# Performance work log

Measured on AMD Instinct MI355X. Metric: run time of the kernel, lower is better.

The kernel has to match this reference:

```python
import jax, jax.numpy as jnp
import numpy as np

D_MODEL = 512; D_STATE = 64; D_CONV = 4; EXPAND = 1; HEADDIM = 128; NGROUPS = 2; CHUNK = 256
D_INNER = EXPAND * (D_MODEL // 2)          # 256
NHEADS = D_INNER // HEADDIM                 # 2
CONV_DIM = D_INNER + 2 * NGROUPS * D_STATE  # 512
D_IN_PROJ = CONV_DIM + NHEADS               # 514

def silu(x):
    return x * jax.nn.sigmoid(x)

def conv1x1(x, w, b):
    # x: (b,c,h,w), w: (o,c)
    return jnp.einsum('bchw,oc->bohw', x, w) + b[None, :, None, None]

def dwconv3x3(x, w, b):
    # depthwise 3x3, SAME padding; w: (c,1,3,3)
    c = x.shape[1]
    y = jax.lax.conv_general_dilated(x, w, (1, 1), 'SAME', feature_group_count=c,
                                     dimension_numbers=('NCHW', 'OIHW', 'NCHW'))
    return y + b[None, :, None, None]

def causal_dwconv1d(x, w, b):
    # x: (b,L,c); w: (c,k). Torch pads k-1 both sides then slices [:L] -> causal left pad.
    k = w.shape[1]
    xp = jnp.pad(x, ((0, 0), (k - 1, 0), (0, 0))).transpose(0, 2, 1)  # (b,c,L+k-1)
    y = jax.lax.conv_general_dilated(xp, w[:, None, :], (1,), 'VALID',
                                     feature_group_count=w.shape[0],
                                     dimension_numbers=('NCH', 'OIH', 'NCH'))
    return y.transpose(0, 2, 1) + b

def axis_attn(x, qw, qb, fw, fb, axis):
    # DualAxisAggAttn single-axis step
    qkv = conv1x1(x, qw, qb)
    c = x.shape[1]
    q, k, v = qkv[:, :1], qkv[:, 1:1 + c], qkv[:, 1 + c:]
    dim = -1 if axis == 'W' else -2
    scores = jax.nn.softmax(q, axis=dim)
    ctx = jnp.sum(k * scores, axis=dim, keepdims=True)
    out = x + jax.nn.sigmoid(v) * ctx
    return conv1x1(out, fw, fb)

def segsum(x):
    # x: (...,T) -> (...,T,T) lower-triangular segment sums, -inf above diagonal
    T = x.shape[-1]
    cs = jnp.cumsum(x, -1)
    d = cs[..., :, None] - cs[..., None, :]
    mask = jnp.tril(jnp.ones((T, T), bool))
    return jnp.where(mask, d, -jnp.inf)

def ssd(X, A, B, C, chunk):
    # Mamba2 SSD chunked scan. X: (b,l,h,p) = x*dt; A: (b,l,h) = dt*A_head; B,C: (b,l,h,n)
    b, l, h, p = X.shape; n = B.shape[-1]; c = l // chunk
    X = X.reshape(b, c, chunk, h, p)
    B = B.reshape(b, c, chunk, h, n)
    C = C.reshape(b, c, chunk, h, n)
    A = A.reshape(b, c, chunk, h).transpose(0, 3, 1, 2)  # (b,h,c,L)
    Acs = jnp.cumsum(A, -1)
    L = jnp.exp(segsum(A))  # (b,h,c,L,L) intra-chunk decay
    Yd = jnp.einsum('bclhn,bcshn,bhcls,bcshp->bclhp', C, B, L, X)
    dec = jnp.exp(Acs[..., -1:] - Acs)
    st = jnp.einsum('bclhn,bhcl,bclhp->bchpn', B, dec, X)  # chunk end-states
    st = jnp.concatenate([jnp.zeros_like(st[:, :1]), st], 1)
    dchunk = jnp.exp(segsum(jnp.pad(Acs[..., -1], ((0, 0), (0, 0), (1, 0)))))
    st = jnp.einsum('bhzc,bchpn->bzhpn', dchunk, st)[:, :-1]  # states entering each chunk
    Yo = jnp.einsum('bclhn,bchpn,bhcl->bclhp', C, st, jnp.exp(Acs))
    return (Yd + Yo).reshape(b, l, h, p)

def setup_inputs() -> dict:
    key = jax.random.key(0)
    ks = jax.random.split(key, 12)
    s = 0.02
    p = {}
    p['u'] = jax.random.normal(ks[0], (8, D_MODEL, 64, 64), jnp.float32)
    p['sc_w1'] = jax.random.normal(ks[1], (D_MODEL, D_MODEL)) * s
    p['sc_b1'] = jnp.zeros((D_MODEL,))
    p['sc_wdw'] = jax.random.normal(ks[2], (D_MODEL, 1, 3, 3)) * s
    p['sc_bdw'] = jnp.zeros((D_MODEL,))
    p['sc_w2'] = jax.random.normal(ks[3], (D_INNER, D_MODEL)) * s
    p['sc_b2'] = jnp.zeros((D_INNER,))
    p['mc_w'] = jax.random.normal(ks[4], (D_INNER, D_MODEL)) * s
    p['mc_b'] = jnp.zeros((D_INNER,))
    p['qkvW_w'] = jax.random.normal(ks[5], (1 + 2 * D_INNER, D_INNER)) * s
    p['qkvW_b'] = jnp.zeros((1 + 2 * D_INNER,))
    p['qkvH_w'] = jax.random.normal(ks[6], (1 + 2 * D_INNER, D_INNER)) * s
    p['qkvH_b'] = jnp.zeros((1 + 2 * D_INNER,))
    p['fuseW_w'] = jax.random.normal(ks[7], (D_INNER, D_INNER)) * s
    p['fuseW_b'] = jnp.zeros((D_INNER,))
    p['fuseH_w'] = jax.random.normal(ks[8], (D_INNER, D_INNER)) * s
    p['fuseH_b'] = jnp.zeros((D_INNER,))
    p['in_proj_w'] = jax.random.normal(ks[9], (D_IN_PROJ, D_INNER)) * s
    p['conv1d_w'] = jax.random.normal(ks[10], (CONV_DIM, D_CONV)) * s
    p['conv1d_b'] = jnp.zeros((CONV_DIM,))
    dt = np.exp(np.linspace(np.log(1e-3), np.log(0.1), NHEADS))
    p['dt_bias'] = jnp.asarray(dt + np.log(-np.expm1(-dt)), jnp.float32)
    p['A_log'] = jnp.asarray(np.log(np.linspace(1.0, 16.0, NHEADS)), jnp.float32)
    p['D'] = jnp.ones((NHEADS,))
    p['norm_w'] = jnp.ones((D_INNER,))
    p['outp_w'] = jax.random.normal(ks[11], (D_MODEL, 2 * D_INNER)) * s
    p['outp_b'] = jnp.zeros((D_MODEL,))
    return p

def reference(u, sc_w1, sc_b1, sc_wdw, sc_bdw, sc_w2, sc_b2, mc_w, mc_b,
              qkvW_w, qkvW_b, qkvH_w, qkvH_b, fuseW_w, fuseW_b, fuseH_w, fuseH_b,
              in_proj_w, conv1d_w, conv1d_b, dt_bias, A_log, D, norm_w, outp_w, outp_b):
    b, _, H, W = u.shape
    # short_conv branch (light_ConvBlock: 1x1 -> dw3x3 -> 1x1, all SiLU; BN folded into bias)
    z = silu(conv1x1(u, sc_w1, sc_b1))
    z = silu(dwconv3x3(z, sc_wdw, sc_bdw))
    z = silu(conv1x1(z, sc_w2, sc_b2))
    # main branch
    x = silu(conv1x1(u, mc_w, mc_b))
    x = axis_attn(x, qkvW_w, qkvW_b, fuseW_w, fuseW_b, 'W')
    x = axis_attn(x, qkvH_w, qkvH_b, fuseH_w, fuseH_b, 'H')
    seqlen = H * W
    u2 = x.transpose(0, 2, 3, 1).reshape(b, seqlen, D_INNER)  # b (h w) c
    xbcdt = u2 @ in_proj_w.T  # (b,l,d_in_proj)
    xBC = xbcdt[..., :CONV_DIM]
    dt = jax.nn.softplus(xbcdt[..., CONV_DIM:] + dt_bias)  # (b,l,h)
    A = -jnp.exp(A_log)  # (h,)
    xBC = silu(causal_dwconv1d(xBC, conv1d_w, conv1d_b))
    xs = xBC[..., :D_INNER]
    Bs = xBC[..., D_INNER:D_INNER + NGROUPS * D_STATE].reshape(b, seqlen, NGROUPS, D_STATE)
    Cs = xBC[..., D_INNER + NGROUPS * D_STATE:].reshape(b, seqlen, NGROUPS, D_STATE)
    Xh = xs.reshape(b, seqlen, NHEADS, HEADDIM)
    rep = NHEADS // NGROUPS
    Bh = jnp.repeat(Bs, rep, axis=2)
    Ch = jnp.repeat(Cs, rep, axis=2)
    y = ssd(Xh * dt[..., None], dt * A[None, None, :], Bh, Ch, CHUNK)
    y = y + Xh * D[None, None, :, None]  # D skip connection
    y = y.reshape(b, seqlen, D_INNER)
    # RMSNormGated with z=None -> plain RMSNorm
    y = y * jax.lax.rsqrt(jnp.mean(y * y, -1, keepdims=True) + 1e-5) * norm_w
    y = y.reshape(b, H, W, D_INNER).transpose(0, 3, 1, 2)
    y = jnp.concatenate([z, y], axis=1)
    return conv1x1(y, outp_w, outp_b)
```

## Files before the change

kernel.cpp:

```cpp
#include <hip/hip_runtime.h>
#include <hip/hip_bf16.h>
#include <cstddef>
#include <cstdint>

#define PTOT 32768
#define HWSZ 4096

typedef __attribute__((ext_vector_type(8))) short bf16x8;
typedef __attribute__((ext_vector_type(4))) short s16x4;
typedef __attribute__((ext_vector_type(4))) float f32x4;

__device__ __forceinline__ float sigf(float x){ return 1.f/(1.f+__expf(-x)); }
__device__ __forceinline__ float siluf(float x){ return x*sigf(x); }
__device__ __forceinline__ short f2b(float x){
  __hip_bfloat16 h = __float2bfloat16(x);
  return *reinterpret_cast<short*>(&h);
}
__device__ __forceinline__ float b2f(short s){
  unsigned u = ((unsigned)(unsigned short)s) << 16;
  return __uint_as_float(u);
}

__device__ __forceinline__ void gload16(const void* g, void* l){
  __builtin_amdgcn_global_load_lds(
      (const __attribute__((address_space(1))) unsigned int*)g,
      (__attribute__((address_space(3))) unsigned int*)l, 16, 0, 0);
}

__global__ __launch_bounds__(256) void k_cvtw(
    const float* __restrict__ s0, const float* __restrict__ s1, const float* __restrict__ s2,
    const float* __restrict__ s3, const float* __restrict__ s4,
    short* __restrict__ dst){
  int idx = blockIdx.x*256 + threadIdx.x;
  const float* s; int off;
  if      (idx <  262144){ s=s0; off=idx; }
  else if (idx <  393216){ s=s1; off=idx- 262144; }
  else if (idx <  524288){ s=s2; off=idx- 393216; }
  else if (idx <  655616){ s=s3; off=idx- 524288; }
  else if (idx <  917760){ s=s4; off=idx- 655616; }
  else return;
  dst[idx] = f2b(s[off]);
}

__global__ __launch_bounds__(256) void k_wcomp(
    const float* __restrict__ qkvHw, const float* __restrict__ fuWw,
    const float* __restrict__ fuWb,  const float* __restrict__ qkvHb,
    const float* __restrict__ inpw,  const float* __restrict__ fuHw,
    const float* __restrict__ fuHb,
    const float* __restrict__ scb1,  const float* __restrict__ mcb,
    short* __restrict__ wcomb, float* __restrict__ bcomb,
    short* __restrict__ wi2,   float* __restrict__ bi2,
    short* __restrict__ wqH,   short* __restrict__ wdt,
    float* __restrict__ bzx)
{
  int blk = blockIdx.x;
  int tid = threadIdx.x;
  __shared__ float as[256];
  __shared__ float red[256];
  if (blk < 513){
    int i = blk;
    int r = (i==512) ? 0 : (i+1);
    as[tid]  = qkvHw[(size_t)r*256 + tid];
    red[tid] = as[tid] * fuWb[tid];
    __syncthreads();
    for (int off=128; off; off>>=1){ if (tid<off) red[tid]+=red[tid+off]; __syncthreads(); }
    float acc = 0.f;
    #pragma unroll 8
    for (int k=0;k<256;k++) acc += as[k]*fuWw[(size_t)k*256 + tid];
    if (i < 512){
      wcomb[(size_t)(256+i)*256 + tid] = f2b(acc);
      if (tid==0) bcomb[256+i] = red[0] + qkvHb[r];
    } else {
      wqH[tid] = f2b(acc);
      if (tid==0) bcomb[768] = red[0] + qkvHb[0];
    }
  } else if (blk < 769){
    int j = blk - 513;
    wcomb[(size_t)j*256 + tid] = f2b(fuWw[(size_t)j*256 + tid]);
    if (tid==0) bcomb[j] = fuWb[j];
  } else if (blk < 1283){
    int j = blk - 769;
    as[tid]  = inpw[(size_t)j*256 + tid];
    red[tid] = as[tid] * fuHb[tid];
    __syncthreads();
    for (int off=128; off; off>>=1){ if (tid<off) red[tid]+=red[tid+off]; __syncthreads(); }
    float acc = 0.f;
    #pragma unroll 8
    for (int k=0;k<256;k++) acc += as[k]*fuHw[(size_t)k*256 + tid];
    if (j < 512){
      wi2[(size_t)j*256 + tid] = f2b(acc);
      if (tid==0) bi2[j] = red[0];
    } else {
      wdt[(size_t)(j-512)*256 + tid] = f2b(acc);
      if (tid==0) bi2[j] = red[0];
    }
  } else {
    int j = (blk - 1283)*256 + tid;
    bzx[j] = (j < 512) ? scb1[j] : mcb[j-512];
  }
}

__global__ __launch_bounds__(256) void k_transpose(const float* __restrict__ in, short* __restrict__ out){
  __shared__ float tile[64][33];
  int b = blockIdx.z;
  int c0 = blockIdx.y * 64;
  int s0 = blockIdx.x * 32;
  int tx = threadIdx.x, ty = threadIdx.y;
  const float* ip = in + ((size_t)b*512 + c0)*HWSZ + s0;
  for (int i = ty; i < 64; i += 8) tile[i][tx] = ip[(size_t)i*HWSZ + tx];
  __syncthreads();
  for (int i = ty; i < 32; i += 8){
    unsigned lo = (unsigned)(unsigned short)f2b(tile[2*tx][i]);
    unsigned hi = (unsigned)(unsigned short)f2b(tile[2*tx+1][i]);
    unsigned pk = lo | (hi<<16);
    *reinterpret_cast<unsigned*>(&out[((size_t)((b<<12) + s0 + i))*512 + c0 + 2*tx]) = pk;
  }
}

template<int ACT, int OUT_NCHW>
__global__ __launch_bounds__(256) void k_gemm(
    const short* __restrict__ A0, const short* __restrict__ A1,
    int kSplit, int lda0, int lda1,
    const short* __restrict__ Wt, const float* __restrict__ bias,
    void* __restrict__ Cpv, int N, int K, int ldc, int qkvPerm,
    short* __restrict__ Cp2, int nSplit2, int ldc2)
{
  __shared__ char arena[17408];
  short* Alds = (short*)arena;
  short* Wlds = (short*)(arena + 8192);

  int tid = threadIdx.x;
  int lane = tid & 63;
  int wv = tid >> 6;
  int wr = wv >> 1, wc = wv & 1;
  int lr = lane & 15, lh = lane >> 4;
  int bm = blockIdx.x * 128;
  int bn = blockIdx.y * 128;

  int rl = lane >> 2;
  int kg = (lane & 3) << 3;

  const short* aB0[2];
  const short* aB1[2];
  const short* wB[2];
  #pragma unroll
  for (int j=0;j<2;j++){
    int r = wv*32 + j*16 + rl;
    int m = bm + r;
    aB0[j] = A0 + (size_t)m*lda0 + kg;
    aB1[j] = A1 + (size_t)m*lda1 + kg;
    int n = bn + r; if (n > N-1) n = N-1;
    int wn = qkvPerm ? (n+1) : n;
    wB[j] = Wt + (size_t)wn*K + kg;
  }

  f32x4 acc[4][4];
  #pragma unroll
  for (int i=0;i<4;i++)
    #pragma unroll
    for (int j=0;j<4;j++) acc[i][j] = (f32x4){0.f,0.f,0.f,0.f};

  for (int k0 = 0; k0 < K; k0 += 32){
    {
      const short* s0;
      const short* s1;
      if (k0 < kSplit){ s0 = aB0[0] + k0; s1 = aB0[1] + k0; }
      else            { s0 = aB1[0] + (k0 - kSplit); s1 = aB1[1] + (k0 - kSplit); }
      gload16(s0, &Alds[(wv*32)*32]);
      gload16(s1, &Alds[(wv*32 + 16)*32]);
      gload16(wB[0] + k0, &Wlds[(wv*32)*32]);
      gload16(wB[1] + k0, &Wlds[(wv*32 + 16)*32]);
    }
    __syncthreads();
    bf16x8 af[4], bfr[4];
    #pragma unroll
    for (int mi=0;mi<4;mi++)
      af[mi] = *reinterpret_cast<const bf16x8*>(&Alds[(wr*64 + mi*16 + lr)*32 + lh*8]);
    #pragma unroll
    for (int ni=0;ni<4;ni++)
      bfr[ni] = *reinterpret_cast<const bf16x8*>(&Wlds[(wc*64 + ni*16 + lr)*32 + lh*8]);
    #pragma unroll
    for (int mi=0;mi<4;mi++)
      #pragma unroll
      for (int ni=0;ni<4;ni++)
        acc[mi][ni] = __builtin_amdgcn_mfma_f32_16x16x32_bf16(af[mi], bfr[ni], acc[mi][ni], 0, 0, 0);
    __syncthreads();
  }

  if (!OUT_NCHW){
    short* Cp = (short*)Cpv;
    #pragma unroll
    for (int mi=0;mi<4;mi++){
      int m = bm + wr*64 + mi*16 + lh*4;
      #pragma unroll
      for (int ni=0;ni<4;ni++){
        int n = bn + wc*64 + ni*16 + lr;
        if (n < N){
          int wn = qkvPerm ? (n+1) : n;
          float bb = bias ? bias[wn] : 0.f;
          #pragma unroll
          for (int r=0;r<4;r++){
            float v = acc[mi][ni][r] + bb;
            if (ACT==1) v = siluf(v);
            short sv = f2b(v);
            if (n < nSplit2) Cp[(size_t)(m+r)*ldc + n] = sv;
            else             Cp2[(size_t)(m+r)*ldc2 + (n - nSplit2)] = sv;
          }
        }
      }
    }
  } else {
    float* Cp = (float*)Cpv;
    float* Sep = ((float*)arena) + wv*16*68;
    #pragma unroll
    for (int mi=0;mi<4;mi++){
      __syncthreads();
      #pragma unroll
      for (int ni=0;ni<4;ni++){
        int n = bn + wc*64 + ni*16 + lr;
        float bb = (bias && n < N) ? bias[n] : 0.f;
        #pragma unroll
        for (int r=0;r<4;r++){
          float v = acc[mi][ni][r] + bb;
          if (ACT==1) v = siluf(v);
          Sep[(lh*4+r)*68 + ni*16 + lr] = v;
        }
      }
      __syncthreads();
      int m = bm + wr*64 + mi*16 + lr;
      size_t mb = ((size_t)(m>>12)*ldc)*HWSZ + (m & 4095);
      #pragma unroll
      for (int g=0; g<16; g++){
        int nl = g*4 + lh;
        float v = Sep[lr*68 + nl];
        int nn = bn + wc*64 + nl;
        if (nn < N) Cp[mb + (size_t)nn*HWSZ] = v;
      }
    }
  }
}

__global__ __launch_bounds__(256) void k_dwconv3x3(const short* __restrict__ in,
    const float* __restrict__ w, const float* __restrict__ bias, short* __restrict__ out){
  int tid = threadIdx.x;
  int cq = tid & 127;
  int wi = tid >> 7;
  int bw = blockIdx.x;
  int b  = bw >> 5;
  int wc = ((bw & 31) << 1) | wi;
  int h0 = blockIdx.y << 4;
  int c  = cq << 2;

  float arr[36];
  {
    const float* wp = &w[c*9];
    #pragma unroll
    for (int t=0;t<9;t++){
      f32x4 v = *reinterpret_cast<const f32x4*>(wp + t*4);
      arr[t*4+0]=v[0]; arr[t*4+1]=v[1]; arr[t*4+2]=v[2]; arr[t*4+3]=v[3];
    }
  }
  f32x4 bias4 = *reinterpret_cast<const f32x4*>(&bias[c]);

  int pb = b << 12;
  auto ldrow = [&](int r, int dw)->f32x4 {
    int ww = wc + dw;
    if ((unsigned)r >= 64u || (unsigned)ww >= 64u) return (f32x4){0.f,0.f,0.f,0.f};
    s16x4 v = *reinterpret_cast<const s16x4*>(&in[((size_t)(pb + (r<<6) + ww) << 9) + c]);
    return (f32x4){b2f(v[0]), b2f(v[1]), b2f(v[2]), b2f(v[3])};
  };

  f32x4 a00,a01,a02,a10,a11,a12,a20,a21,a22;
  a00=ldrow(h0-1,-1); a01=ldrow(h0-1,0); a02=ldrow(h0-1,1);
  a10=ldrow(h0  ,-1); a11=ldrow(h0  ,0); a12=ldrow(h0  ,1);
  #pragma unroll
  for (int hh=0; hh<16; hh++){
    int h = h0 + hh;
    a20=ldrow(h+1,-1); a21=ldrow(h+1,0); a22=ldrow(h+1,1);
    s16x4 o;
    #pragma unroll
    for (int j=0;j<4;j++){
      float v = bias4[j];
      v = fmaf(a00[j], arr[j*9+0], v);
      v = fmaf(a01[j], arr[j*9+1], v);
      v = fmaf(a02[j], arr[j*9+2], v);
      v = fmaf(a10[j], arr[j*9+3], v);
      v = fmaf(a11[j], arr[j*9+4], v);
      v = fmaf(a12[j], arr[j*9+5], v);
      v = fmaf(a20[j], arr[j*9+6], v);
      v = fmaf(a21[j], arr[j*9+7], v);
      v = fmaf(a22[j], arr[j*9+8], v);
      o[j] = f2b(siluf(v));
    }
    *reinterpret_cast<s16x4*>(&out[((size_t)(pb + (h<<6) + wc) << 9) + c]) = o;
    a00=a10; a01=a11; a02=a12;
    a10=a20; a11=a21; a12=a22;
  }
}

__global__ __launch_bounds__(256) void k_attn_ctx(
    const short* __restrict__ xq, int xqld, const short* __restrict__ wq, const float* __restrict__ bq,
    const short* __restrict__ qkv, int qld, int kOff,
    float* __restrict__ ctx, int axisH){
  int bl = blockIdx.x;
  int b = bl >> 6, line = bl & 63;
  int tid = threadIdx.x;
  int pbase = b << 12;
  __shared__ float qs[64], es[64];
  __shared__ float qpart[4][64];
  __shared__ float part[8][260];
  auto pos = [&](int t)->int { return axisH ? (pbase | (t<<6) | line) : (pbase | (line<<6) | t); };
  {
    int t = tid & 63, qr = tid >> 6;
    const short* xp = &xq[(size_t)pos(t)*xqld + qr*64];
    const short* wp = &wq[qr*64];
    float pq = 0.f;
    #pragma unroll
    for (int j=0;j<8;j++){
      bf16x8 xv = *reinterpret_cast<const bf16x8*>(xp + j*8);
      bf16x8 wv = *reinterpret_cast<const bf16x8*>(wp + j*8);
      #pragma unroll
      for (int e=0;e<8;e++) pq = fmaf(b2f(xv[e]), b2f(wv[e]), pq);
    }
    qpart[qr][t] = pq;
  }
  __syncthreads();
  if (tid < 64) qs[tid] = bq[0] + qpart[0][tid] + qpart[1][tid] + qpart[2][tid] + qpart[3][tid];
  __syncthreads();
  float mx = -1e30f;
  for (int t=0;t<64;t++) mx = fmaxf(mx, qs[t]);
  if (tid < 64) es[tid] = __expf(qs[tid]-mx);
  __syncthreads();
  int tg = tid >> 5;
  int cg = tid & 31;
  float pacc[8];
  #pragma unroll
  for (int j=0;j<8;j++) pacc[j]=0.f;
  #pragma unroll
  for (int tt=0; tt<8; tt++){
    int t = tg*8 + tt;
    bf16x8 kv = *reinterpret_cast<const bf16x8*>(&qkv[(size_t)pos(t)*qld + kOff + cg*8]);
    float e = es[t];
    #pragma unroll
    for (int j=0;j<8;j++) pacc[j] = fmaf(e, b2f(kv[j]), pacc[j]);
  }
  #pragma unroll
  for (int j=0;j<8;j++) part[tg][cg*8+j] = pacc[j];
  __syncthreads();
  float s = 0.f;
  for (int t=0;t<64;t++) s += es[t];
  float inv = 1.f/s;
  int c = tid;
  float v = 0.f;
  #pragma unroll
  for (int g=0; g<8; g++) v += part[g][c];
  ctx[(size_t)bl*256 + c] = v*inv;
}

__global__ __launch_bounds__(256) void k_attn_apply(const short* __restrict__ x, int xld,
    const short* __restrict__ qkv, int qld, int vOff, const float* __restrict__ ctx,
    short* __restrict__ out, int axisH){
  int idx = blockIdx.x*256 + threadIdx.x;
  int p = idx >> 5;
  int c0 = (idx & 31) << 3;
  int line = axisH ? (p & 63) : ((p >> 6) & 63);
  int bl = (p >> 12)*64 + line;
  bf16x8 vv = *reinterpret_cast<const bf16x8*>(&qkv[(size_t)p*qld + vOff + c0]);
  bf16x8 xv = *reinterpret_cast<const bf16x8*>(&x[(size_t)p*xld + c0]);
  const float* cp = &ctx[(size_t)bl*256 + c0];
  bf16x8 o;
  #pragma unroll
  for (int j=0;j<8;j++)
    o[j] = f2b(b2f(xv[j]) + sigf(b2f(vv[j]))*cp[j]);
  *reinterpret_cast<bf16x8*>(&out[(size_t)p*256 + c0]) = o;
}

__global__ __launch_bounds__(256) void k_dt(const short* __restrict__ xwh,
    const short* __restrict__ wdt, const float* __restrict__ bdt,
    const float* __restrict__ dt_bias, float* __restrict__ dtb){
  int tid = threadIdx.x, lane = tid & 63, wv = tid >> 6;
  int p = blockIdx.x*4 + wv;
  s16x4 xv = *reinterpret_cast<const s16x4*>(&xwh[(size_t)p*256 + lane*4]);
  s16x4 w0 = *reinterpret_cast<const s16x4*>(&wdt[lane*4]);
  s16x4 w1 = *reinterpret_cast<const s16x4*>(&wdt[256 + lane*4]);
  float d0 = 0.f, d1 = 0.f;
  #pragma unroll
  for (int j=0;j<4;j++){
    float xf = b2f(xv[j]);
    d0 = fmaf(xf, b2f(w0[j]), d0);
    d1 = fmaf(xf, b2f(w1[j]), d1);
  }
  #pragma unroll
  for (int off=32; off; off>>=1){ d0 += __shfl_down(d0, off); d1 += __shfl_down(d1, off); }
  if (lane == 0){
    float x0 = d0 + bdt[0] + dt_bias[0];
    float x1 = d1 + bdt[1] + dt_bias[1];
    dtb[(size_t)p*2 + 0] = (x0 > 20.f) ? x0 : log1pf(__expf(x0));
    dtb[(size_t)p*2 + 1] = (x1 > 20.f) ? x1 : log1pf(__expf(x1));
  }
}

__global__ __launch_bounds__(256) void k_conv1d(const short* __restrict__ xbc_in,
    const float* __restrict__ w, const float* __restrict__ bias, short* __restrict__ xBC){
  int tid = threadIdx.x;
  int cq = tid & 127;
  int c  = cq << 2;
  int half = tid >> 7;
  int bs = blockIdx.x;
  int b  = bs >> 7;
  int t0 = ((((bs & 127) << 1) | half) << 4);

  float wk[16];
  {
    const float* wp = &w[c*4];
    #pragma unroll
    for (int t=0;t<4;t++){
      f32x4 v = *reinterpret_cast<const f32x4*>(wp + t*4);
      wk[t*4+0]=v[0]; wk[t*4+1]=v[1]; wk[t*4+2]=v[2]; wk[t*4+3]=v[3];
    }
  }
  f32x4 bias4 = *reinterpret_cast<const f32x4*>(&bias[c]);

  int pb = b << 12;
  auto ld = [&](int t)->f32x4 {
    if (t < 0) return (f32x4){0.f,0.f,0.f,0.f};
    s16x4 v = *reinterpret_cast<const s16x4*>(&xbc_in[((size_t)(pb + t) << 9) + c]);
    return (f32x4){b2f(v[0]), b2f(v[1]), b2f(v[2]), b2f(v[3])};
  };

  f32x4 x0,x1,x2,x3;
  x0 = ld(t0-3); x1 = ld(t0-2); x2 = ld(t0-1);
  #pragma unroll
  for (int tt=0; tt<16; tt++){
    int t = t0 + tt;
    x3 = ld(t);
    s16x4 o;
    #pragma unroll
    for (int j=0;j<4;j++){
      float v = bias4[j];
      v = fmaf(x0[j], wk[j*4+0], v);
      v = fmaf(x1[j], wk[j*4+1], v);
      v = fmaf(x2[j], wk[j*4+2], v);
      v = fmaf(x3[j], wk[j*4+3], v);
      o[j] = f2b(siluf(v));
    }
    *reinterpret_cast<s16x4*>(&xBC[((size_t)(pb + t) << 9) + c]) = o;
    x0=x1; x1=x2; x2=x3;
  }
}

__global__ __launch_bounds__(256) void k_ssd_states(
  const short* __restrict__ xBC, const float* __restrict__ dtb, const float* __restrict__ A_log,
  float* __restrict__ states, float* __restrict__ AcsG, float* __restrict__ AtotG)
{
  int ci = blockIdx.x, h = blockIdx.y, b = blockIdx.z;
  int tid = threadIdx.x, lane = tid & 63, wv = tid >> 6;
  int lg = lane >> 4, lr = lane & 15;
  __shared__ float sa[256], sb[256];
  __shared__ short Bt[64*72];
  __shared__ short Xt[128*72];
  int base = (b<<12) | (ci<<8);
  float Ah = -__expf(A_log[h]);
  sa[tid] = dtb[(size_t)(base + tid)*2 + h] * Ah;
  __syncthreads();
  float* src = sa; float* dst = sb;
  for (int off=1; off<256; off<<=1){
    float v = src[tid];
    if (tid >= off) v += src[tid - off];
    dst[tid] = v;
    __syncthreads();
    float* tswap = src; src = dst; dst = tswap;
  }
  float acs = src[tid];
  float atot = src[255];
  AcsG[((size_t)((b*2+h)*16 + ci))*256 + tid] = acs;
  if (tid == 0) AtotG[(b*2+h)*16 + ci] = atot;

  f32x4 acc[8];
  #pragma unroll
  for (int pf=0;pf<8;pf++) acc[pf] = (f32x4){0.f,0.f,0.f,0.f};

  for (int t0=0; t0<256; t0+=64){
    __syncthreads();
    {
      int t = tid >> 2;
      int n0 = (tid & 3) << 4;
      float d = __expf(atot - src[t0 + t]);
      const short* sp = &xBC[(size_t)(base + t0 + t)*512 + 256 + (h<<6) + n0];
      bf16x8 v0 = *reinterpret_cast<const bf16x8*>(sp);
      bf16x8 v1 = *reinterpret_cast<const bf16x8*>(sp+8);
      #pragma unroll
      for (int e=0;e<8;e++) Bt[(n0+e)*72 + t]   = f2b(b2f(v0[e])*d);
      #pragma unroll
      for (int e=0;e<8;e++) Bt[(n0+8+e)*72 + t] = f2b(b2f(v1[e])*d);
    }
    {
      int t = tid >> 2;
      int p0 = (tid & 3) << 5;
      float dtv = dtb[(size_t)(base + t0 + t)*2 + h];
      const short* sp = &xBC[(size_t)(base + t0 + t)*512 + (h<<7) + p0];
      #pragma unroll
      for (int q=0;q<4;q++){
        bf16x8 v = *reinterpret_cast<const bf16x8*>(sp + q*8);
        #pragma unroll
        for (int e=0;e<8;e++) Xt[(p0 + q*8 + e)*72 + t] = f2b(b2f(v[e])*dtv);
      }
    }
    __syncthreads();
    #pragma unroll
    for (int kk=0; kk<2; kk++){
      bf16x8 af = *reinterpret_cast<const bf16x8*>(&Bt[(wv*16 + lr)*72 + kk*32 + lg*8]);
      #pragma unroll
      for (int pf=0;pf<8;pf++){
        bf16x8 xf = *reinterpret_cast<const bf16x8*>(&Xt[(pf*16 + lr)*72 + kk*32 + lg*8]);
        acc[pf] = __builtin_amdgcn_mfma_f32_16x16x32_bf16(af, xf, acc[pf], 0, 0, 0);
      }
    }
  }
  float* stp = states + (((size_t)(b*16+ci)*2 + h) << 13);
  #pragma unroll
  for (int pf=0;pf<8;pf++){
    #pragma unroll
    for (int r=0;r<4;r++)
      stp[(wv*16 + lg*4 + r)*128 + pf*16 + lr] = acc[pf][r];
  }
}

__global__ __launch_bounds__(256) void k_ssd_scan(const float* __restrict__ states,
    const float* __restrict__ AtotG, float* __restrict__ R){
  int bh = blockIdx.x;
  int b = bh >> 1, h = bh & 1;
  int tid = threadIdx.x;
  float r[32];
  #pragma unroll
  for (int j=0;j<32;j++) r[j]=0.f;
  for (int ci=0; ci<16; ci++){
    size_t off = (((size_t)(b*16+ci)*2) + h) << 13;
    #pragma unroll
    for (int j=0;j<32;j++) R[off + tid + (j<<8)] = r[j];
    if (ci < 15){
      float sc = __expf(AtotG[bh*16 + ci]);
      #pragma unroll
      for (int j=0;j<32;j++) r[j] = fmaf(sc, r[j], states[off + tid + (j<<8)]);
    }
  }
}

__global__ __launch_bounds__(256) void k_ssd_y_norm(
  const short* __restrict__ xBC, const float* __restrict__ dtb,
  const float* __restrict__ AcsG, const float* __restrict__ R,
  const float* __restrict__ Dp, const float* __restrict__ nw, short* __restrict__ ynorm)
{
// ... 61 lines not shown
        bf16x8 bb0 = *reinterpret_cast<const bf16x8*>(&Bbf[(f*16+lr)*72 + lg*8]);
        bf16x8 bb1 = *reinterpret_cast<const bf16x8*>(&Bbf[(f*16+lr)*72 + 32 + lg*8]);
        sacc[f] = __builtin_amdgcn_mfma_f32_16x16x32_bf16(ca0, bb0, sacc[f], 0, 0, 0);
        sacc[f] = __builtin_amdgcn_mfma_f32_16x16x32_bf16(ca1, bb1, sacc[f], 0, 0, 0);
      }
      #pragma unroll
      for (int f=0;f<4;f++){
        #pragma unroll
        for (int r=0;r<4;r++){
          int ll = w*16 + lg*4 + r;
          int ss = f*16 + lr;
          float v = 0.f;
          if (s0 + ss <= l0 + ll)
            v = sacc[f][r] * __expf(acs_l[ll] - acs_s[ss]) * dt_s[ss];
          Sbf[ll*72 + ss] = f2b(v);
        }
      }
      __syncthreads();

      bf16x8 sa0 = *reinterpret_cast<const bf16x8*>(&Sbf[(w*16+lr)*72 + lg*8]);
      bf16x8 sa1 = *reinterpret_cast<const bf16x8*>(&Sbf[(w*16+lr)*72 + 32 + lg*8]);
      #pragma unroll
      for (int pf=0;pf<8;pf++){
        bf16x8 x0 = *reinterpret_cast<const bf16x8*>(&Xt[(pf*16+lr)*76 + lg*8]);
        bf16x8 x1 = *reinterpret_cast<const bf16x8*>(&Xt[(pf*16+lr)*76 + 32 + lg*8]);
        yacc[pf] = __builtin_amdgcn_mfma_f32_16x16x32_bf16(sa0, x0, yacc[pf], 0, 0, 0);
        yacc[pf] = __builtin_amdgcn_mfma_f32_16x16x32_bf16(sa1, x1, yacc[pf], 0, 0, 0);
      }
    }

    __syncthreads();
    {
      size_t roff = (((size_t)(b*16+ci)*2) + h) << 13;
      int n = tid >> 2;
      const float* src = R + roff + (size_t)n*128;
      #pragma unroll
      for (int j=0;j<8;j++){
        int p = ((tid & 3) << 2) + (j << 4);
        float4 f = *reinterpret_cast<const float4*>(&src[p]);
        Xt[(p+0)*76 + n] = f2b(f.x);
        Xt[(p+1)*76 + n] = f2b(f.y);
        Xt[(p+2)*76 + n] = f2b(f.z);
        Xt[(p+3)*76 + n] = f2b(f.w);
      }
    }
    __syncthreads();
    f32x4 racc[8];
    #pragma unroll
    for (int pf=0;pf<8;pf++) racc[pf] = (f32x4){0.f,0.f,0.f,0.f};
    {
      bf16x8 ca0 = *reinterpret_cast<const bf16x8*>(&Cbf[(w*16+lr)*72 + lg*8]);
      bf16x8 ca1 = *reinterpret_cast<const bf16x8*>(&Cbf[(w*16+lr)*72 + 32 + lg*8]);
      #pragma unroll
      for (int pf=0;pf<8;pf++){
        bf16x8 x0 = *reinterpret_cast<const bf16x8*>(&Xt[(pf*16+lr)*76 + lg*8]);
        bf16x8 x1 = *reinterpret_cast<const bf16x8*>(&Xt[(pf*16+lr)*76 + 32 + lg*8]);
        racc[pf] = __builtin_amdgcn_mfma_f32_16x16x32_bf16(ca0, x0, racc[pf], 0, 0, 0);
        racc[pf] = __builtin_amdgcn_mfma_f32_16x16x32_bf16(ca1, x1, racc[pf], 0, 0, 0);
      }
    }
    float Dh = Dp[h];
    float el[4];
    #pragma unroll
    for (int r=0;r<4;r++) el[r] = __expf(acs_l[w*16 + lg*4 + r]);
    #pragma unroll
    for (int pf=0;pf<8;pf++){
      f32x4 o;
      #pragma unroll
      for (int r=0;r<4;r++){
        int ll = w*16 + lg*4 + r;
        int p = pf*16 + lr;
        size_t pix = (size_t)(base + l0 + ll);
        float xraw = b2f(xBC[pix*512 + (h<<7) + p]);
        o[r] = yacc[pf][r] + el[r]*racc[pf][r] + Dh*xraw;
      }
      yv[pf] = o;
    }
  };

  f32x4 y0[8], y1[8];
  body(0, y0);
  body(1, y1);

  f32x4 ss = (f32x4){0.f,0.f,0.f,0.f};
  #pragma unroll
  for (int pf=0;pf<8;pf++){
    #pragma unroll
    for (int r=0;r<4;r++)
      ss[r] += y0[pf][r]*y0[pf][r] + y1[pf][r]*y1[pf][r];
  }
  #pragma unroll
  for (int m=1; m<16; m<<=1){
    #pragma unroll
    for (int r=0;r<4;r++) ss[r] += __shfl_xor(ss[r], m);
  }
  f32x4 scale;
  #pragma unroll
  for (int r=0;r<4;r++) scale[r] = rsqrtf(ss[r]*(1.f/256.f) + 1e-5f);

  #pragma unroll
  for (int pf=0;pf<8;pf++){
    float nw0 = nw[pf*16 + lr];
    float nw1 = nw[128 + pf*16 + lr];
    #pragma unroll
    for (int r=0;r<4;r++){
      size_t pix = (size_t)(base + l0 + w*16 + lg*4 + r);
      ynorm[pix*256 + pf*16 + lr]        = f2b(y0[pf][r]*scale[r]*nw0);
      ynorm[pix*256 + 128 + pf*16 + lr]  = f2b(y1[pf][r]*scale[r]*nw1);
    }
  }
}

extern "C" void kernel_launch(void* const* d_in, const int* in_sizes, int n_in,
                              void* d_out, int out_size, void* d_ws, size_t ws_size,
                              hipStream_t stream)
{
  (void)in_sizes; (void)n_in; (void)out_size; (void)ws_size;
  const float* u        = (const float*)d_in[0];
  const float* sc_w1    = (const float*)d_in[1];
  const float* sc_b1    = (const float*)d_in[2];
  const float* sc_wdw   = (const float*)d_in[3];
  const float* sc_bdw   = (const float*)d_in[4];
  const float* sc_w2    = (const float*)d_in[5];
  const float* sc_b2    = (const float*)d_in[6];
  const float* mc_w     = (const float*)d_in[7];
  const float* mc_b     = (const float*)d_in[8];
  const float* qkvW_w   = (const float*)d_in[9];
  const float* qkvW_b   = (const float*)d_in[10];
  const float* qkvH_w   = (const float*)d_in[11];
  const float* qkvH_b   = (const float*)d_in[12];
  const float* fuseW_w  = (const float*)d_in[13];
  const float* fuseW_b  = (const float*)d_in[14];
  const float* fuseH_w  = (const float*)d_in[15];
  const float* fuseH_b  = (const float*)d_in[16];
  const float* in_proj_w= (const float*)d_in[17];
  const float* conv1d_w = (const float*)d_in[18];
  const float* conv1d_b = (const float*)d_in[19];
  const float* dt_bias  = (const float*)d_in[20];
  const float* A_log    = (const float*)d_in[21];
  const float* Dp       = (const float*)d_in[22];
  const float* norm_w   = (const float*)d_in[23];
  const float* outp_w   = (const float*)d_in[24];
  const float* outp_b   = (const float*)d_in[25];

  char* wsb = (char*)d_ws;
  size_t off = 0;
  auto alloc = [&](size_t bytes){ void* p = wsb + off; off = (off + bytes + 255) & ~(size_t)255; return p; };
  short* wbf   = (short*)alloc((size_t)1247000*2);
  float* bcomb = (float*)alloc(769*4);
  float* bi2   = (float*)alloc(514*4);
  float* bzx   = (float*)alloc(768*4);
  short* slotB = (short*)alloc((size_t)PTOT*768*2);
  short* slotC = (short*)alloc((size_t)PTOT*512*2);
  short* slotZ = (short*)alloc((size_t)PTOT*256*2);
  short* slotE = (short*)alloc((size_t)PTOT*256*2);
  short* slotF = (short*)alloc((size_t)PTOT*256*2);
  float* slotS = (float*)alloc((size_t)4460000*4);

  float* dtb     = slotS;
  float* AcsG    = slotS + 65536;
  float* AtotG   = slotS + 131072;
  float* statesB = slotS + 131328;
  float* Rb      = slotS + 131328 + 2097152;
  float* ctxb    = slotS;
  short* ynorm   = slotE;
  short* xwh     = slotF;

  short* w_zx   = wbf + 0;
  short* w_sc2  = wbf + 393216;
  short* w_qkvW = wbf + 524288;
  short* w_outp = wbf + 655616;
  short* wcomb  = wbf + 917760;
  short* wi2    = wbf + 1114368;
  short* wqH    = wbf + 1245440;
  short* wdt    = wbf + 1245696;

  short* u_pm = (short*)d_out;
  float* out  = (float*)d_out;

  const int BIG = 1<<30;

  k_cvtw<<<3585, 256, 0, stream>>>(sc_w1, mc_w, sc_w2, qkvW_w, outp_w, wbf);
  k_wcomp<<<1286, 256, 0, stream>>>(qkvH_w, fuseW_w, fuseW_b, qkvH_b, in_proj_w, fuseH_w, fuseH_b,
                                    sc_b1, mc_b, wcomb, bcomb, wi2, bi2, wqH, wdt, bzx);
  k_transpose<<<dim3(128,8,8), dim3(32,8), 0, stream>>>(u, u_pm);

  k_gemm<1,0><<<dim3(256,6), 256, 0, stream>>>(u_pm, u_pm, BIG, 512, 512, w_zx, bzx,
                                               slotB, 768, 512, 512, 0, slotE, 512, 256);
  k_dwconv3x3<<<dim3(256,4), 256, 0, stream>>>(slotB, sc_wdw, sc_bdw, slotC);
  k_gemm<1,0><<<dim3(256,2), 256, 0, stream>>>(slotC, slotC, BIG, 512, 512, w_sc2, sc_b2,
                                               slotZ, 256, 512, 256, 0, nullptr, BIG, 0);

  k_gemm<0,0><<<dim3(256,4), 256, 0, stream>>>(slotE, slotE, BIG, 256, 256, w_qkvW, qkvW_b,
                                               slotB, 512, 256, 512, 1, nullptr, BIG, 0);
  k_attn_ctx<<<512, 256, 0, stream>>>(slotE, 256, w_qkvW, qkvW_b, slotB, 512, 0, ctxb, 0);
  k_attn_apply<<<4096, 256, 0, stream>>>(slotE, 256, slotB, 512, 256, ctxb, xwh, 0);
  k_gemm<0,0><<<dim3(256,6), 256, 0, stream>>>(xwh, xwh, BIG, 256, 256, wcomb, bcomb,
                                               slotB, 768, 256, 768, 0, nullptr, BIG, 0);
  k_attn_ctx<<<512, 256, 0, stream>>>(xwh, 256, wqH, bcomb + 768, slotB, 768, 256, ctxb, 1);
  k_attn_apply<<<4096, 256, 0, stream>>>(slotB, 768, slotB, 768, 512, ctxb, xwh, 1);
  k_gemm<0,0><<<dim3(256,4), 256, 0, stream>>>(xwh, xwh, BIG, 256, 256, wi2, bi2,
                                               slotB, 512, 256, 512, 0, nullptr, BIG, 0);
  k_dt<<<8192, 256, 0, stream>>>(xwh, wdt, bi2 + 512, dt_bias, dtb);
  k_conv1d<<<1024, 256, 0, stream>>>(slotB, conv1d_w, conv1d_b, slotC);

  k_ssd_states<<<dim3(16,2,8), 256, 0, stream>>>(slotC, dtb, A_log, statesB, AcsG, AtotG);
  k_ssd_scan<<<16, 256, 0, stream>>>(statesB, AtotG, Rb);
  k_ssd_y_norm<<<dim3(64,8), 256, 0, stream>>>(slotC, dtb, AcsG, Rb, Dp, norm_w, ynorm);

  k_gemm<0,1><<<dim3(256,4), 256, 0, stream>>>(slotZ, ynorm, 256, 256, 256, w_outp, outp_b,
                                               out, 512, 512, 512, 0, nullptr, BIG, 0);
}
```

Measured before the change: 468.3 us.

## Merge independent kernels into horizontally fused launches to cut launch count

```diff
diff --git a/kernel.cpp b/kernel.cpp
--- a/kernel.cpp
+++ b/kernel.cpp
@@ -27,22 +27,9 @@
       (__attribute__((address_space(3))) unsigned int*)l, 16, 0, 0);
 }
 
-__global__ __launch_bounds__(256) void k_cvtw(
+__global__ __launch_bounds__(256) void k_initw(
     const float* __restrict__ s0, const float* __restrict__ s1, const float* __restrict__ s2,
-    const float* __restrict__ s3, const float* __restrict__ s4,
-    short* __restrict__ dst){
-  int idx = blockIdx.x*256 + threadIdx.x;
-  const float* s; int off;
-  if      (idx <  262144){ s=s0; off=idx; }
-  else if (idx <  393216){ s=s1; off=idx- 262144; }
-  else if (idx <  524288){ s=s2; off=idx- 393216; }
-  else if (idx <  655616){ s=s3; off=idx- 524288; }
-  else if (idx <  917760){ s=s4; off=idx- 655616; }
-  else return;
-  dst[idx] = f2b(s[off]);
-}
-
-__global__ __launch_bounds__(256) void k_wcomp(
+    const float* __restrict__ s3, const float* __restrict__ s4, short* __restrict__ dst,
     const float* __restrict__ qkvHw, const float* __restrict__ fuWw,
     const float* __restrict__ fuWb,  const float* __restrict__ qkvHb,
     const float* __restrict__ inpw,  const float* __restrict__ fuHw,
@@ -53,10 +40,22 @@
     short* __restrict__ wqH,   short* __restrict__ wdt,
     float* __restrict__ bzx)
 {
-  int blk = blockIdx.x;
   int tid = threadIdx.x;
   __shared__ float as[256];
   __shared__ float red[256];
+  if (blockIdx.x < 3585){
+    int idx = blockIdx.x*256 + tid;
+    const float* s; int off;
+    if      (idx <  262144){ s=s0; off=idx; }
+    else if (idx <  393216){ s=s1; off=idx- 262144; }
+    else if (idx <  524288){ s=s2; off=idx- 393216; }
+    else if (idx <  655616){ s=s3; off=idx- 524288; }
+    else if (idx <  917760){ s=s4; off=idx- 655616; }
+    else return;
+    dst[idx] = f2b(s[off]);
+    return;
+  }
+  int blk = blockIdx.x - 3585;
   if (blk < 513){
     int i = blk;
     int r = (i==512) ? 0 : (i+1);
@@ -240,61 +239,325 @@
   }
 }
 
-__global__ __launch_bounds__(256) void k_dwconv3x3(const short* __restrict__ in,
-    const float* __restrict__ w, const float* __restrict__ bias, short* __restrict__ out){
+__global__ __launch_bounds__(256) void k_gemm_dwconv(
+    const short* __restrict__ Agm, const short* __restrict__ Wt, const float* __restrict__ bias,
+    short* __restrict__ Cp,
+    const short* __restrict__ din, const float* __restrict__ dw, const float* __restrict__ db,
+    short* __restrict__ dout)
+{
+  __shared__ __align__(16) char arena[17408];
+  int id = blockIdx.x;
   int tid = threadIdx.x;
-  int cq = tid & 127;
-  int wi = tid >> 7;
-  int bw = blockIdx.x;
-  int b  = bw >> 5;
-  int wc = ((bw & 31) << 1) | wi;
-  int h0 = blockIdx.y << 4;
-  int c  = cq << 2;
-
-  float arr[36];
-  {
-    const float* wp = &w[c*9];
-    #pragma unroll
-    for (int t=0;t<9;t++){
-      f32x4 v = *reinterpret_cast<const f32x4*>(wp + t*4);
-      arr[t*4+0]=v[0]; arr[t*4+1]=v[1]; arr[t*4+2]=v[2]; arr[t*4+3]=v[3];
-    }
-  }
-  f32x4 bias4 = *reinterpret_cast<const f32x4*>(&bias[c]);
-
-  int pb = b << 12;
-  auto ldrow = [&](int r, int dw)->f32x4 {
-    int ww = wc + dw;
-    if ((unsigned)r >= 64u || (unsigned)ww >= 64u) return (f32x4){0.f,0.f,0.f,0.f};
-    s16x4 v = *reinterpret_cast<const s16x4*>(&in[((size_t)(pb + (r<<6) + ww) << 9) + c]);
-    return (f32x4){b2f(v[0]), b2f(v[1]), b2f(v[2]), b2f(v[3])};
-  };
-
-  f32x4 a00,a01,a02,a10,a11,a12,a20,a21,a22;
-  a00=ldrow(h0-1,-1); a01=ldrow(h0-1,0); a02=ldrow(h0-1,1);
-  a10=ldrow(h0  ,-1); a11=ldrow(h0  ,0); a12=ldrow(h0  ,1);
-  #pragma unroll
-  for (int hh=0; hh<16; hh++){
-    int h = h0 + hh;
-    a20=ldrow(h+1,-1); a21=ldrow(h+1,0); a22=ldrow(h+1,1);
-    s16x4 o;
+  if (id < 1024){
+    short* Alds = (short*)arena;
+    short* Wlds = (short*)(arena + 8192);
+    int lane = tid & 63, wv = tid >> 6;
+    int wr = wv >> 1, wc = wv & 1;
+    int lr = lane & 15, lh = lane >> 4;
+    int bm = (id & 255) * 128, bn = (id >> 8) * 128;
+    int rl = lane >> 2, kg = (lane & 3) << 3;
+    const short* aB[2]; const short* wB[2];
+    #pragma unroll
+    for (int j=0;j<2;j++){
+      int r = wv*32 + j*16 + rl;
+      aB[j] = Agm + (size_t)(bm+r)*256 + kg;
+      wB[j] = Wt + (size_t)(bn+r+1)*256 + kg;
+    }
+    f32x4 acc[4][4];
+    #pragma unroll
+    for (int i=0;i<4;i++)
+      #pragma unroll
+      for (int j=0;j<4;j++) acc[i][j] = (f32x4){0.f,0.f,0.f,0.f};
+    for (int k0 = 0; k0 < 256; k0 += 32){
+      gload16(aB[0]+k0, &Alds[(wv*32)*32]);
+      gload16(aB[1]+k0, &Alds[(wv*32+16)*32]);
+      gload16(wB[0]+k0, &Wlds[(wv*32)*32]);
+      gload16(wB[1]+k0, &Wlds[(wv*32+16)*32]);
+      __syncthreads();
+      bf16x8 af[4], bfr[4];
+      #pragma unroll
+      for (int mi=0;mi<4;mi++)
+        af[mi] = *reinterpret_cast<const bf16x8*>(&Alds[(wr*64 + mi*16 + lr)*32 + lh*8]);
+      #pragma unroll
+      for (int ni=0;ni<4;ni++)
+        bfr[ni] = *reinterpret_cast<const bf16x8*>(&Wlds[(wc*64 + ni*16 + lr)*32 + lh*8]);
+      #pragma unroll
+      for (int mi=0;mi<4;mi++)
+        #pragma unroll
+        for (int ni=0;ni<4;ni++)
+          acc[mi][ni] = __builtin_amdgcn_mfma_f32_16x16x32_bf16(af[mi], bfr[ni], acc[mi][ni], 0, 0, 0);
+      __syncthreads();
+    }
+    #pragma unroll
+    for (int mi=0;mi<4;mi++){
+      int m = bm + wr*64 + mi*16 + lh*4;
+      #pragma unroll
+      for (int ni=0;ni<4;ni++){
+        int n = bn + wc*64 + ni*16 + lr;
+        float bb = bias[n+1];
+        #pragma unroll
+        for (int r=0;r<4;r++)
+          Cp[(size_t)(m+r)*512 + n] = f2b(acc[mi][ni][r] + bb);
+      }
+    }
+  } else {
+    int id2 = id - 1024;
+    int bw = id2 & 255, hy = id2 >> 8;
+    int cq = tid & 127;
+    int wi = tid >> 7;
+    int b  = bw >> 5;
+    int wc = ((bw & 31) << 1) | wi;
+    int h0 = hy << 4;
+    int c  = cq << 2;
+    float arr[36];
+    {
+      const float* wp = &dw[c*9];
+      #pragma unroll
+      for (int t=0;t<9;t++){
+        f32x4 v = *reinterpret_cast<const f32x4*>(wp + t*4);
+        arr[t*4+0]=v[0]; arr[t*4+1]=v[1]; arr[t*4+2]=v[2]; arr[t*4+3]=v[3];
+      }
+    }
+    f32x4 bias4 = *reinterpret_cast<const f32x4*>(&db[c]);
+    int pb = b << 12;
+    auto ldrow = [&](int r, int dwo)->f32x4 {
+      int ww = wc + dwo;
+      if ((unsigned)r >= 64u || (unsigned)ww >= 64u) return (f32x4){0.f,0.f,0.f,0.f};
+      s16x4 v = *reinterpret_cast<const s16x4*>(&din[((size_t)(pb + (r<<6) + ww) << 9) + c]);
+      return (f32x4){b2f(v[0]), b2f(v[1]), b2f(v[2]), b2f(v[3])};
+    };
+    f32x4 a00,a01,a02,a10,a11,a12,a20,a21,a22;
+    a00=ldrow(h0-1,-1); a01=ldrow(h0-1,0); a02=ldrow(h0-1,1);
+    a10=ldrow(h0  ,-1); a11=ldrow(h0  ,0); a12=ldrow(h0  ,1);
+    #pragma unroll
+    for (int hh=0; hh<16; hh++){
+      int h = h0 + hh;
+      a20=ldrow(h+1,-1); a21=ldrow(h+1,0); a22=ldrow(h+1,1);
+      s16x4 o;
+      #pragma unroll
+      for (int j=0;j<4;j++){
+        float v = bias4[j];
+        v = fmaf(a00[j], arr[j*9+0], v);
+        v = fmaf(a01[j], arr[j*9+1], v);
+        v = fmaf(a02[j], arr[j*9+2], v);
+        v = fmaf(a10[j], arr[j*9+3], v);
+        v = fmaf(a11[j], arr[j*9+4], v);
+        v = fmaf(a12[j], arr[j*9+5], v);
+        v = fmaf(a20[j], arr[j*9+6], v);
+        v = fmaf(a21[j], arr[j*9+7], v);
+        v = fmaf(a22[j], arr[j*9+8], v);
+        o[j] = f2b(siluf(v));
+      }
+      *reinterpret_cast<s16x4*>(&dout[((size_t)(pb + (h<<6) + wc) << 9) + c]) = o;
+      a00=a10; a01=a11; a02=a12;
+      a10=a20; a11=a21; a12=a22;
+    }
+  }
+}
+
+__global__ __launch_bounds__(256) void k_gemm_ctx(
+    const short* __restrict__ Agm, const short* __restrict__ Wt, const float* __restrict__ bias,
+    short* __restrict__ Cp,
+    const short* __restrict__ xq, const short* __restrict__ wq, const float* __restrict__ bq,
+    const short* __restrict__ kvb, float* __restrict__ ctx)
+{
+  __shared__ __align__(16) char arena[17408];
+  int id = blockIdx.x;
+  int tid = threadIdx.x;
+  if (id < 512){
+    short* Alds = (short*)arena;
+    short* Wlds = (short*)(arena + 8192);
+    int lane = tid & 63, wv = tid >> 6;
+    int wr = wv >> 1, wc = wv & 1;
+    int lr = lane & 15, lh = lane >> 4;
+    int bm = (id & 255) * 128, bn = (id >> 8) * 128;
+    int rl = lane >> 2, kg = (lane & 3) << 3;
+    const short* aB[2]; const short* wB[2];
+    #pragma unroll
+    for (int j=0;j<2;j++){
+      int r = wv*32 + j*16 + rl;
+      aB[j] = Agm + (size_t)(bm+r)*512 + kg;
+      int n = bn + r; if (n > 255) n = 255;
+      wB[j] = Wt + (size_t)n*512 + kg;
+    }
+    f32x4 acc[4][4];
+    #pragma unroll
+    for (int i=0;i<4;i++)
+      #pragma unroll
+      for (int j=0;j<4;j++) acc[i][j] = (f32x4){0.f,0.f,0.f,0.f};
+    for (int k0 = 0; k0 < 512; k0 += 32){
+      gload16(aB[0]+k0, &Alds[(wv*32)*32]);
+      gload16(aB[1]+k0, &Alds[(wv*32+16)*32]);
+      gload16(wB[0]+k0, &Wlds[(wv*32)*32]);
+      gload16(wB[1]+k0, &Wlds[(wv*32+16)*32]);
+      __syncthreads();
+      bf16x8 af[4], bfr[4];
+      #pragma unroll
+      for (int mi=0;mi<4;mi++)
+        af[mi] = *reinterpret_cast<const bf16x8*>(&Alds[(wr*64 + mi*16 + lr)*32 + lh*8]);
+      #pragma unroll
+      for (int ni=0;ni<4;ni++)
+        bfr[ni] = *reinterpret_cast<const bf16x8*>(&Wlds[(wc*64 + ni*16 + lr)*32 + lh*8]);
+      #pragma unroll
+      for (int mi=0;mi<4;mi++)
+        #pragma unroll
+        for (int ni=0;ni<4;ni++)
+          acc[mi][ni] = __builtin_amdgcn_mfma_f32_16x16x32_bf16(af[mi], bfr[ni], acc[mi][ni], 0, 0, 0);
+      __syncthreads();
+    }
+    #pragma unroll
+    for (int mi=0;mi<4;mi++){
+      int m = bm + wr*64 + mi*16 + lh*4;
+      #pragma unroll
+      for (int ni=0;ni<4;ni++){
+        int n = bn + wc*64 + ni*16 + lr;
+        if (n < 256){
+          float bb = bias[n];
+          #pragma unroll
+          for (int r=0;r<4;r++)
+            Cp[(size_t)(m+r)*256 + n] = f2b(siluf(acc[mi][ni][r] + bb));
+        }
+      }
+    }
+  } else {
+    float* qs    = (float*)arena;
+    float* es    = qs + 64;
+    float* qpart = es + 64;
+    float* part  = qpart + 256;
+    int bl = id - 512;
+    int b = bl >> 6, line = bl & 63;
+    int pbase = b << 12;
+    auto pos = [&](int t)->int { return (pbase | (line<<6) | t); };
+    {
+      int t = tid & 63, qr = tid >> 6;
+      const short* xp = &xq[(size_t)pos(t)*256 + qr*64];
+      const short* wp = &wq[qr*64];
+      float pq = 0.f;
+      #pragma unroll
+      for (int j=0;j<8;j++){
+        bf16x8 xv = *reinterpret_cast<const bf16x8*>(xp + j*8);
+        bf16x8 wv = *reinterpret_cast<const bf16x8*>(wp + j*8);
+        #pragma unroll
+        for (int e=0;e<8;e++) pq = fmaf(b2f(xv[e]), b2f(wv[e]), pq);
+      }
+      qpart[qr*64 + t] = pq;
+    }
+    __syncthreads();
+    if (tid < 64) qs[tid] = bq[0] + qpart[tid] + qpart[64+tid] + qpart[128+tid] + qpart[192+tid];
+    __syncthreads();
+    float mx = -1e30f;
+    for (int t=0;t<64;t++) mx = fmaxf(mx, qs[t]);
+    if (tid < 64) es[tid] = __expf(qs[tid]-mx);
+    __syncthreads();
+    int tg = tid >> 5;
+    int cg = tid & 31;
+    float pacc[8];
+    #pragma unroll
+    for (int j=0;j<8;j++) pacc[j]=0.f;
+    #pragma unroll
+    for (int tt=0; tt<8; tt++){
+      int t = tg*8 + tt;
+      bf16x8 kv = *reinterpret_cast<const bf16x8*>(&kvb[(size_t)pos(t)*512 + cg*8]);
+      float e = es[t];
+      #pragma unroll
+      for (int j=0;j<8;j++) pacc[j] = fmaf(e, b2f(kv[j]), pacc[j]);
+    }
+    #pragma unroll
+    for (int j=0;j<8;j++) part[tg*260 + cg*8+j] = pacc[j];
+    __syncthreads();
+    float s = 0.f;
+    for (int t=0;t<64;t++) s += es[t];
+    float inv = 1.f/s;
+    int c = tid;
+    float v = 0.f;
+    #pragma unroll
+    for (int g=0; g<8; g++) v += part[g*260 + c];
+    ctx[(size_t)bl*256 + c] = v*inv;
+  }
+}
+
+__global__ __launch_bounds__(256) void k_gemm_dt(
+    const short* __restrict__ Agm, const short* __restrict__ Wt, const float* __restrict__ bias,
+    short* __restrict__ Cp,
+    const short* __restrict__ xwh, const short* __restrict__ wdt, const float* __restrict__ bdt,
+    const float* __restrict__ dt_bias, float* __restrict__ dtb)
+{
+  __shared__ __align__(16) char arena[17408];
+  int id = blockIdx.x;
+  int tid = threadIdx.x;
+  if (id < 1024){
+    short* Alds = (short*)arena;
+    short* Wlds = (short*)(arena + 8192);
+    int lane = tid & 63, wv = tid >> 6;
+    int wr = wv >> 1, wc = wv & 1;
+    int lr = lane & 15, lh = lane >> 4;
+    int bm = (id & 255) * 128, bn = (id >> 8) * 128;
+    int rl = lane >> 2, kg = (lane & 3) << 3;
+    const short* aB[2]; const short* wB[2];
+    #pragma unroll
+    for (int j=0;j<2;j++){
+      int r = wv*32 + j*16 + rl;
+      aB[j] = Agm + (size_t)(bm+r)*256 + kg;
+      wB[j] = Wt + (size_t)(bn+r)*256 + kg;
+    }
+    f32x4 acc[4][4];
+    #pragma unroll
+    for (int i=0;i<4;i++)
+      #pragma unroll
+      for (int j=0;j<4;j++) acc[i][j] = (f32x4){0.f,0.f,0.f,0.f};
+    for (int k0 = 0; k0 < 256; k0 += 32){
+      gload16(aB[0]+k0, &Alds[(wv*32)*32]);
+      gload16(aB[1]+k0, &Alds[(wv*32+16)*32]);
+      gload16(wB[0]+k0, &Wlds[(wv*32)*32]);
+      gload16(wB[1]+k0, &Wlds[(wv*32+16)*32]);
+      __syncthreads();
+      bf16x8 af[4], bfr[4];
+      #pragma unroll
+      for (int mi=0;mi<4;mi++)
+        af[mi] = *reinterpret_cast<const bf16x8*>(&Alds[(wr*64 + mi*16 + lr)*32 + lh*8]);
+      #pragma unroll
+      for (int ni=0;ni<4;ni++)
+        bfr[ni] = *reinterpret_cast<const bf16x8*>(&Wlds[(wc*64 + ni*16 + lr)*32 + lh*8]);
+      #pragma unroll
+      for (int mi=0;mi<4;mi++)
+        #pragma unroll
+        for (int ni=0;ni<4;ni++)
+          acc[mi][ni] = __builtin_amdgcn_mfma_f32_16x16x32_bf16(af[mi], bfr[ni], acc[mi][ni], 0, 0, 0);
+      __syncthreads();
+    }
+    #pragma unroll
+    for (int mi=0;mi<4;mi++){
+      int m = bm + wr*64 + mi*16 + lh*4;
+      #pragma unroll
+      for (int ni=0;ni<4;ni++){
+        int n = bn + wc*64 + ni*16 + lr;
+        float bb = bias[n];
+        #pragma unroll
+        for (int r=0;r<4;r++)
+          Cp[(size_t)(m+r)*512 + n] = f2b(acc[mi][ni][r] + bb);
+      }
+    }
+  } else {
+    int lane = tid & 63, wv = tid >> 6;
+    int p = (id - 1024)*4 + wv;
+    s16x4 xv = *reinterpret_cast<const s16x4*>(&xwh[(size_t)p*256 + lane*4]);
+    s16x4 w0 = *reinterpret_cast<const s16x4*>(&wdt[lane*4]);
+    s16x4 w1 = *reinterpret_cast<const s16x4*>(&wdt[256 + lane*4]);
+    float d0 = 0.f, d1 = 0.f;
     #pragma unroll
     for (int j=0;j<4;j++){
-      float v = bias4[j];
-      v = fmaf(a00[j], arr[j*9+0], v);
-      v = fmaf(a01[j], arr[j*9+1], v);
-      v = fmaf(a02[j], arr[j*9+2], v);
-      v = fmaf(a10[j], arr[j*9+3], v);
-      v = fmaf(a11[j], arr[j*9+4], v);
-      v = fmaf(a12[j], arr[j*9+5], v);
-      v = fmaf(a20[j], arr[j*9+6], v);
-      v = fmaf(a21[j], arr[j*9+7], v);
-      v = fmaf(a22[j], arr[j*9+8], v);
-      o[j] = f2b(siluf(v));
-    }
-    *reinterpret_cast<s16x4*>(&out[((size_t)(pb + (h<<6) + wc) << 9) + c]) = o;
-    a00=a10; a01=a11; a02=a12;
-    a10=a20; a11=a21; a12=a22;
+      float xf = b2f(xv[j]);
+      d0 = fmaf(xf, b2f(w0[j]), d0);
+      d1 = fmaf(xf, b2f(w1[j]), d1);
+    }
+    #pragma unroll
+    for (int off=32; off; off>>=1){ d0 += __shfl_down(d0, off); d1 += __shfl_down(d1, off); }
+    if (lane == 0){
+      float x0 = d0 + bdt[0] + dt_bias[0];
+      float x1 = d1 + bdt[1] + dt_bias[1];
+      dtb[(size_t)p*2 + 0] = (x0 > 20.f) ? x0 : log1pf(__expf(x0));
+      dtb[(size_t)p*2 + 1] = (x1 > 20.f) ? x1 : log1pf(__expf(x1));
+    }
   }
 }
 
@@ -373,31 +636,6 @@
   for (int j=0;j<8;j++)
     o[j] = f2b(b2f(xv[j]) + sigf(b2f(vv[j]))*cp[j]);
   *reinterpret_cast<bf16x8*>(&out[(size_t)p*256 + c0]) = o;
-}
-
-__global__ __launch_bounds__(256) void k_dt(const short* __restrict__ xwh,
-    const short* __restrict__ wdt, const float* __restrict__ bdt,
-    const float* __restrict__ dt_bias, float* __restrict__ dtb){
-  int tid = threadIdx.x, lane = tid & 63, wv = tid >> 6;
-  int p = blockIdx.x*4 + wv;
-  s16x4 xv = *reinterpret_cast<const s16x4*>(&xwh[(size_t)p*256 + lane*4]);
-  s16x4 w0 = *reinterpret_cast<const s16x4*>(&wdt[lane*4]);
-  s16x4 w1 = *reinterpret_cast<const s16x4*>(&wdt[256 + lane*4]);
-  float d0 = 0.f, d1 = 0.f;
-  #pragma unroll
-  for (int j=0;j<4;j++){
-    float xf = b2f(xv[j]);
-    d0 = fmaf(xf, b2f(w0[j]), d0);
-    d1 = fmaf(xf, b2f(w1[j]), d1);
-  }
-  #pragma unroll
-  for (int off=32; off; off>>=1){ d0 += __shfl_down(d0, off); d1 += __shfl_down(d1, off); }
-  if (lane == 0){
-    float x0 = d0 + bdt[0] + dt_bias[0];
-    float x1 = d1 + bdt[1] + dt_bias[1];
-    dtb[(size_t)p*2 + 0] = (x0 > 20.f) ? x0 : log1pf(__expf(x0));
-    dtb[(size_t)p*2 + 1] = (x1 > 20.f) ? x1 : log1pf(__expf(x1));
-  }
 }
 
 __global__ __launch_bounds__(256) void k_conv1d(const short* __restrict__ xbc_in,
@@ -765,6 +1003,7 @@
   float* bzx   = (float*)alloc(768*4);
   short* slotB = (short*)alloc((size_t)PTOT*768*2);
   short* slotC = (short*)alloc((size_t)PTOT*512*2);
+  short* slotG = (short*)alloc((size_t)PTOT*512*2);
   short* slotZ = (short*)alloc((size_t)PTOT*256*2);
   short* slotE = (short*)alloc((size_t)PTOT*256*2);
   short* slotF = (short*)alloc((size_t)PTOT*256*2);
@@ -793,28 +1032,25 @@
 
   const int BIG = 1<<30;
 
-  k_cvtw<<<3585, 256, 0, stream>>>(sc_w1, mc_w, sc_w2, qkvW_w, outp_w, wbf);
-  k_wcomp<<<1286, 256, 0, stream>>>(qkvH_w, fuseW_w, fuseW_b, qkvH_b, in_proj_w, fuseH_w, fuseH_b,
+  k_initw<<<4871, 256, 0, stream>>>(sc_w1, mc_w, sc_w2, qkvW_w, outp_w, wbf,
+                                    qkvH_w, fuseW_w, fuseW_b, qkvH_b, in_proj_w, fuseH_w, fuseH_b,
                                     sc_b1, mc_b, wcomb, bcomb, wi2, bi2, wqH, wdt, bzx);
   k_transpose<<<dim3(128,8,8), dim3(32,8), 0, stream>>>(u, u_pm);
 
   k_gemm<1,0><<<dim3(256,6), 256, 0, stream>>>(u_pm, u_pm, BIG, 512, 512, w_zx, bzx,
                                                slotB, 768, 512, 512, 0, slotE, 512, 256);
-  k_dwconv3x3<<<dim3(256,4), 256, 0, stream>>>(slotB, sc_wdw, sc_bdw, slotC);
-  k_gemm<1,0><<<dim3(256,2), 256, 0, stream>>>(slotC, slotC, BIG, 512, 512, w_sc2, sc_b2,
-                                               slotZ, 256, 512, 256, 0, nullptr, BIG, 0);
-
-  k_gemm<0,0><<<dim3(256,4), 256, 0, stream>>>(slotE, slotE, BIG, 256, 256, w_qkvW, qkvW_b,
-                                               slotB, 512, 256, 512, 1, nullptr, BIG, 0);
-  k_attn_ctx<<<512, 256, 0, stream>>>(slotE, 256, w_qkvW, qkvW_b, slotB, 512, 0, ctxb, 0);
-  k_attn_apply<<<4096, 256, 0, stream>>>(slotE, 256, slotB, 512, 256, ctxb, xwh, 0);
+
+  k_gemm_dwconv<<<2048, 256, 0, stream>>>(slotE, w_qkvW, qkvW_b, slotG,
+                                          slotB, sc_wdw, sc_bdw, slotC);
+  k_gemm_ctx<<<1024, 256, 0, stream>>>(slotC, w_sc2, sc_b2, slotZ,
+                                       slotE, w_qkvW, qkvW_b, slotG, ctxb);
+  k_attn_apply<<<4096, 256, 0, stream>>>(slotE, 256, slotG, 512, 256, ctxb, xwh, 0);
   k_gemm<0,0><<<dim3(256,6), 256, 0, stream>>>(xwh, xwh, BIG, 256, 256, wcomb, bcomb,
                                                slotB, 768, 256, 768, 0, nullptr, BIG, 0);
   k_attn_ctx<<<512, 256, 0, stream>>>(xwh, 256, wqH, bcomb + 768, slotB, 768, 256, ctxb, 1);
   k_attn_apply<<<4096, 256, 0, stream>>>(slotB, 768, slotB, 768, 512, ctxb, xwh, 1);
-  k_gemm<0,0><<<dim3(256,4), 256, 0, stream>>>(xwh, xwh, BIG, 256, 256, wi2, bi2,
-                                               slotB, 512, 256, 512, 0, nullptr, BIG, 0);
-  k_dt<<<8192, 256, 0, stream>>>(xwh, wdt, bi2 + 512, dt_bias, dtb);
+  k_gemm_dt<<<9216, 256, 0, stream>>>(xwh, wi2, bi2, slotB,
+                                      xwh, wdt, bi2 + 512, dt_bias, dtb);
   k_conv1d<<<1024, 256, 0, stream>>>(slotB, conv1d_w, conv1d_b, slotC);
 
   k_ssd_states<<<dim3(16,2,8), 256, 0, stream>>>(slotC, dtb, A_log, statesB, AcsG, AtotG);
```

Measured after the change: 561.9 us. +20.0%, slower.
